# Kernel tuning notes

Hardware: AMD Instinct MI355X
Metric: run time of the kernel (lower is better)

## Reference

```python
import jax, jax.numpy as jnp
import numpy as np

B, H, W, C = 8, 50, 50, 256
N_ROIS = 256
ROI_SIZE = 28  # >= pool grid so every bin is non-empty


def setup_inputs() -> dict:
    key = jax.random.key(0)
    k1, k2, k3, k4 = jax.random.split(key, 4)
    feat = jax.random.normal(k1, (B, H, W, C), dtype=jnp.float32)
    batch_idx = jax.random.randint(k2, (N_ROIS,), 0, B)
    x1 = jax.random.randint(k3, (N_ROIS,), 0, W - ROI_SIZE + 1)
    y1 = jax.random.randint(k4, (N_ROIS,), 0, H - ROI_SIZE + 1)
    # rois: (image_index, x1, y1, x2, y2), inclusive coordinates
    rois = jnp.stack([batch_idx, x1, y1, x1 + ROI_SIZE - 1, y1 + ROI_SIZE - 1], axis=1).astype(jnp.int32)
    return {"feat": feat, "rois": rois, "pool_height": 7, "pool_width": 7}


def _roi_max_pool(feat, rois, ph, pw):
    n = rois.shape[0]
    h, w = feat.shape[1], feat.shape[2]
    c = feat.shape[3]
    img, x1, y1, x2, y2 = (rois[:, i] for i in range(5))
    roi_h = (y2 - y1 + 1)  # [N]
    roi_w = (x2 - x1 + 1)

    # Per-pixel bin assignment (adaptive partition): bin = floor(offset * pool / extent)
    dy = jnp.arange(h)[None, :] - y1[:, None]                      # [N,H]
    dx = jnp.arange(w)[None, :] - x1[:, None]                      # [N,W]
    row_bin = jnp.minimum(dy * ph // roi_h[:, None], ph - 1)       # [N,H]
    col_bin = jnp.minimum(dx * pw // roi_w[:, None], pw - 1)       # [N,W]
    row_ok = (dy >= 0) & (dy < roi_h[:, None])
    col_ok = (dx >= 0) & (dx < roi_w[:, None])

    valid = row_ok[:, :, None] & col_ok[:, None, :]                # [N,H,W]
    bin_id = row_bin[:, :, None] * pw + col_bin[:, None, :]        # [N,H,W]
    seg = jnp.arange(n)[:, None, None] * (ph * pw) + bin_id
    dump = n * ph * pw  # junk segment for out-of-ROI pixels
    seg = jnp.where(valid, seg, dump)

    feat_n = feat[img]                                             # [N,H,W,C] gather per ROI
    out = jax.ops.segment_max(
        feat_n.reshape(n * h * w, c), seg.reshape(n * h * w),
        num_segments=n * ph * pw + 1,
    )[: n * ph * pw]
    return out.reshape(n, ph, pw, c)                               # [N,ph,pw,C]


def reference(feat, rois, pool_height, pool_width):
    return _roi_max_pool(feat, rois, int(pool_height), int(pool_width))
```

## Files before the change

kernel.cpp:

```cpp
#include <hip/hip_runtime.h>

constexpr int Hf = 50, Wf = 50, Cf = 256;
constexpr int PH = 7, PW = 7;
constexpr int C4 = Cf / 4;
constexpr int NXCD = 8;

__global__ __launch_bounds__(256) void sort_rois_kernel(
    const int* __restrict__ rois, int n_rois, int n_images,
    int* __restrict__ order) {
  __shared__ int cnt[64];
  __shared__ int base[64];
  for (int i = threadIdx.x; i < n_images; i += blockDim.x) cnt[i] = 0;
  __syncthreads();
  for (int t = threadIdx.x; t < n_rois; t += blockDim.x)
    atomicAdd(&cnt[rois[t * 5]], 1);
  __syncthreads();
  if (threadIdx.x == 0) {
    int acc = 0;
    for (int i = 0; i < n_images; ++i) { base[i] = acc; acc += cnt[i]; }
  }
  __syncthreads();
  for (int t = threadIdx.x; t < n_rois; t += blockDim.x) {
    int slot = atomicAdd(&base[rois[t * 5]], 1);
    order[slot] = t;
  }
}

__global__ __launch_bounds__(256) void roipool_kernel(
    const float4* __restrict__ feat,
    const int*    __restrict__ rois,
    const int*    __restrict__ order,
    float4*       __restrict__ out,
    int n_bins, int q, int rr) {
  int i   = blockIdx.x;
  int xcd = i % NXCD;
  int w   = (xcd < rr ? xcd * (q + 1) : rr * (q + 1) + (xcd - rr) * q)
          + i / NXCD;

  int p = w * 4 + (threadIdx.x >> 6);
  if (p >= n_bins) return;
  int lane = threadIdx.x & 63;

  int s  = p / (PH * PW);
  int rb = p - s * (PH * PW);
  int n  = order[s];
  int py = rb / PW;
  int px = rb - py * PW;

  const int* roi = rois + n * 5;
  int img = roi[0];
  int x1  = roi[1];
  int y1  = roi[2];
  int x2  = roi[3];
  int y2  = roi[4];
  int roi_h = y2 - y1 + 1;
  int roi_w = x2 - x1 + 1;

  int hs = (py * roi_h + PH - 1) / PH;
  int he = ((py + 1) * roi_h + PH - 1) / PH;
  int ws = (px * roi_w + PW - 1) / PW;
  int we = ((px + 1) * roi_w + PW - 1) / PW;

  const float4* fb = feat + (size_t)img * (Hf * Wf * C4) + lane;

  float4 m = make_float4(-INFINITY, -INFINITY, -INFINITY, -INFINITY);

  if (he - hs == 4 && we - ws == 4) {
    const float4* p0 = fb + (size_t)(y1 + hs) * (Wf * C4) + (size_t)(x1 + ws) * C4;
#pragma unroll
    for (int dy = 0; dy < 4; ++dy) {
      const float4* prow = p0 + (size_t)dy * (Wf * C4);
#pragma unroll
      for (int dx = 0; dx < 4; ++dx) {
        float4 v = prow[(size_t)dx * C4];
        m.x = fmaxf(m.x, v.x);
        m.y = fmaxf(m.y, v.y);
        m.z = fmaxf(m.z, v.z);
        m.w = fmaxf(m.w, v.w);
      }
    }
  } else {
    for (int dy = hs; dy < he; ++dy) {
      int y = y1 + dy;
      const float4* prow = fb + (size_t)y * (Wf * C4);
      for (int dx = ws; dx < we; ++dx) {
        int x = x1 + dx;
        float4 v = prow[(size_t)x * C4];
        m.x = fmaxf(m.x, v.x);
        m.y = fmaxf(m.y, v.y);
        m.z = fmaxf(m.z, v.z);
        m.w = fmaxf(m.w, v.w);
      }
    }
  }

  out[((size_t)n * (PH * PW) + rb) * C4 + lane] = m;
}

extern "C" void kernel_launch(void* const* d_in, const int* in_sizes, int n_in,
                              void* d_out, int out_size, void* d_ws, size_t ws_size,
                              hipStream_t stream) {
  const float* feat = (const float*)d_in[0];
  const int*   rois = (const int*)d_in[1];
  int n_rois   = in_sizes[1] / 5;
  int n_images = in_sizes[0] / (Hf * Wf * Cf);
  int n_bins   = n_rois * PH * PW;
  int blocks   = (n_bins + 3) / 4;
  int q  = blocks / NXCD;
  int rr = blocks % NXCD;

  int* order = (int*)d_ws;

  sort_rois_kernel<<<1, 256, 0, stream>>>(rois, n_rois, n_images, order);
  roipool_kernel<<<blocks, 256, 0, stream>>>(
      (const float4*)feat, rois, order, (float4*)d_out, n_bins, q, rr);
}
```

Before: 84.37 us.

## Assign blocks per image with grid-stride bins and packed sorted ROI metadata

```diff
diff --git a/kernel.cpp b/kernel.cpp
--- a/kernel.cpp
+++ b/kernel.cpp
@@ -1,15 +1,17 @@
 #include <hip/hip_runtime.h>
 
 constexpr int Hf = 50, Wf = 50, Cf = 256;
-constexpr int PH = 7, PW = 7;
+constexpr int PH = 7, PW = 7, NB = PH * PW;
 constexpr int C4 = Cf / 4;
 constexpr int NXCD = 8;
 
+typedef float f32x4 __attribute__((ext_vector_type(4)));
+
 __global__ __launch_bounds__(256) void sort_rois_kernel(
     const int* __restrict__ rois, int n_rois, int n_images,
-    int* __restrict__ order) {
-  __shared__ int cnt[64];
-  __shared__ int base[64];
+    int* __restrict__ hdr,
+    int4* __restrict__ meta) {
+  __shared__ int cnt[64], base[64];
   for (int i = threadIdx.x; i < n_images; i += blockDim.x) cnt[i] = 0;
   __syncthreads();
   for (int t = threadIdx.x; t < n_rois; t += blockDim.x)
@@ -17,84 +19,89 @@
   __syncthreads();
   if (threadIdx.x == 0) {
     int acc = 0;
-    for (int i = 0; i < n_images; ++i) { base[i] = acc; acc += cnt[i]; }
+    for (int i = 0; i < n_images; ++i) {
+      base[i] = acc;
+      hdr[i] = cnt[i];
+      hdr[n_images + i] = acc;
+      acc += cnt[i];
+    }
   }
   __syncthreads();
   for (int t = threadIdx.x; t < n_rois; t += blockDim.x) {
-    int slot = atomicAdd(&base[rois[t * 5]], 1);
-    order[slot] = t;
+    const int* r = rois + t * 5;
+    int slot = atomicAdd(&base[r[0]], 1);
+    meta[2 * slot]     = make_int4(r[0], r[1], r[2], t);
+    meta[2 * slot + 1] = make_int4(r[3], r[4], 0, 0);
   }
 }
 
-__global__ __launch_bounds__(256) void roipool_kernel(
+__global__ __launch_bounds__(256) void pool_kernel(
     const float4* __restrict__ feat,
-    const int*    __restrict__ rois,
-    const int*    __restrict__ order,
+    const int*    __restrict__ hdr,
+    const int4*   __restrict__ meta,
     float4*       __restrict__ out,
-    int n_bins, int q, int rr) {
-  int i   = blockIdx.x;
-  int xcd = i % NXCD;
-  int w   = (xcd < rr ? xcd * (q + 1) : rr * (q + 1) + (xcd - rr) * q)
-          + i / NXCD;
+    int n_images, int bpi) {
+  int j = blockIdx.x % n_images;
+  int t = blockIdx.x / n_images;
+  int cnt    = hdr[j];
+  int sbase  = hdr[n_images + j];
+  int nb_img = cnt * NB;
+  int lane = threadIdx.x & 63;
+  int wv   = threadIdx.x >> 6;
 
-  int p = w * 4 + (threadIdx.x >> 6);
-  if (p >= n_bins) return;
-  int lane = threadIdx.x & 63;
+  for (int lb = t * 4 + wv; lb < nb_img; lb += bpi * 4) {
+    int q  = lb / NB;
+    int rb = lb - q * NB;
+    int s  = sbase + q;
 
-  int s  = p / (PH * PW);
-  int rb = p - s * (PH * PW);
-  int n  = order[s];
-  int py = rb / PW;
-  int px = rb - py * PW;
+    int4 m0 = meta[2 * s];
+    int4 m1 = meta[2 * s + 1];
+    int img = m0.x, x1 = m0.y, y1 = m0.z, n = m0.w;
+    int roi_h = m1.y - y1 + 1;
+    int roi_w = m1.x - x1 + 1;
 
-  const int* roi = rois + n * 5;
-  int img = roi[0];
-  int x1  = roi[1];
-  int y1  = roi[2];
-  int x2  = roi[3];
-  int y2  = roi[4];
-  int roi_h = y2 - y1 + 1;
-  int roi_w = x2 - x1 + 1;
+    int py = rb / PW;
+    int px = rb - py * PW;
 
-  int hs = (py * roi_h + PH - 1) / PH;
-  int he = ((py + 1) * roi_h + PH - 1) / PH;
-  int ws = (px * roi_w + PW - 1) / PW;
-  int we = ((px + 1) * roi_w + PW - 1) / PW;
+    const float4* fb = feat + (size_t)img * (Hf * Wf * C4) + lane;
+    float4 m = make_float4(-INFINITY, -INFINITY, -INFINITY, -INFINITY);
 
-  const float4* fb = feat + (size_t)img * (Hf * Wf * C4) + lane;
-
-  float4 m = make_float4(-INFINITY, -INFINITY, -INFINITY, -INFINITY);
-
-  if (he - hs == 4 && we - ws == 4) {
-    const float4* p0 = fb + (size_t)(y1 + hs) * (Wf * C4) + (size_t)(x1 + ws) * C4;
+    if (roi_h == 28 && roi_w == 28) {
+      const float4* p0 = fb + (size_t)(y1 + 4 * py) * (Wf * C4)
+                            + (size_t)(x1 + 4 * px) * C4;
 #pragma unroll
-    for (int dy = 0; dy < 4; ++dy) {
-      const float4* prow = p0 + (size_t)dy * (Wf * C4);
+      for (int dy = 0; dy < 4; ++dy) {
+        const float4* prow = p0 + (size_t)dy * (Wf * C4);
 #pragma unroll
-      for (int dx = 0; dx < 4; ++dx) {
-        float4 v = prow[(size_t)dx * C4];
-        m.x = fmaxf(m.x, v.x);
-        m.y = fmaxf(m.y, v.y);
-        m.z = fmaxf(m.z, v.z);
-        m.w = fmaxf(m.w, v.w);
+        for (int dx = 0; dx < 4; ++dx) {
+          float4 v = prow[(size_t)dx * C4];
+          m.x = fmaxf(m.x, v.x);
+          m.y = fmaxf(m.y, v.y);
+          m.z = fmaxf(m.z, v.z);
+          m.w = fmaxf(m.w, v.w);
+        }
+      }
+    } else {
+      int hs = (py * roi_h + PH - 1) / PH;
+      int he = ((py + 1) * roi_h + PH - 1) / PH;
+      int ws = (px * roi_w + PW - 1) / PW;
+      int we = ((px + 1) * roi_w + PW - 1) / PW;
+      for (int dy = hs; dy < he; ++dy) {
+        const float4* prow = fb + (size_t)(y1 + dy) * (Wf * C4);
+        for (int dx = ws; dx < we; ++dx) {
+          float4 v = prow[(size_t)(x1 + dx) * C4];
+          m.x = fmaxf(m.x, v.x);
+          m.y = fmaxf(m.y, v.y);
+          m.z = fmaxf(m.z, v.z);
+          m.w = fmaxf(m.w, v.w);
+        }
       }
     }
-  } else {
-    for (int dy = hs; dy < he; ++dy) {
-      int y = y1 + dy;
-      const float4* prow = fb + (size_t)y * (Wf * C4);
-      for (int dx = ws; dx < we; ++dx) {
-        int x = x1 + dx;
-        float4 v = prow[(size_t)x * C4];
-        m.x = fmaxf(m.x, v.x);
-        m.y = fmaxf(m.y, v.y);
-        m.z = fmaxf(m.z, v.z);
-        m.w = fmaxf(m.w, v.w);
-      }
-    }
+
+    f32x4 val = {m.x, m.y, m.z, m.w};
+    __builtin_nontemporal_store(
+        val, (f32x4*)(out + ((size_t)n * NB + rb) * C4 + lane));
   }
-
-  out[((size_t)n * (PH * PW) + rb) * C4 + lane] = m;
 }
 
 extern "C" void kernel_launch(void* const* d_in, const int* in_sizes, int n_in,
@@ -104,14 +111,16 @@
   const int*   rois = (const int*)d_in[1];
   int n_rois   = in_sizes[1] / 5;
   int n_images = in_sizes[0] / (Hf * Wf * Cf);
-  int n_bins   = n_rois * PH * PW;
-  int blocks   = (n_bins + 3) / 4;
-  int q  = blocks / NXCD;
-  int rr = blocks % NXCD;
+  if (n_images < 1) n_images = 1;
 
-  int* order = (int*)d_ws;
+  int*  hdr  = (int*)d_ws;
+  int4* meta = (int4*)((char*)d_ws + 256);
 
-  sort_rois_kernel<<<1, 256, 0, stream>>>(rois, n_rois, n_images, order);
-  roipool_kernel<<<blocks, 256, 0, stream>>>(
-      (const float4*)feat, rois, order, (float4*)d_out, n_bins, q, rr);
+  sort_rois_kernel<<<1, 256, 0, stream>>>(rois, n_rois, n_images, hdr, meta);
+
+  int avg  = (n_rois + n_images - 1) / n_images;
+  int bpi  = (2 * avg * NB + 3) / 4;
+  int blocks = n_images * bpi;
+  pool_kernel<<<blocks, 256, 0, stream>>>(
+      (const float4*)feat, hdr, meta, (float4*)d_out, n_images, bpi);
 }
```

Result: no change. 83.70 us (median of 2 runs) (-0.8%).
